# Optimization experiments

Hardware: AMD Instinct MI355X
Metric: run time of the kernel (lower is better)

Reference implementation:

```python
import jax, jax.numpy as jnp
import numpy as np


def _ramp_filter(H):
    # skimage-style Fourier ramp filter: 2*|f| with f = fftfreq(H)
    f = np.fft.fftfreq(H)
    return (2.0 * np.abs(f)).astype(np.float32)


def setup_inputs() -> dict:
    key = jax.random.key(0)
    N, H_in, W_in, D_out = 8, 768, 360, 512
    radon_image = jax.random.normal(key, (N, 1, H_in, W_in), dtype=jnp.float32)
    hG = jnp.asarray(_ramp_filter(H_in)).reshape(1, 1, H_in, 1)
    return {"radon_image": radon_image, "hG": hG, "D_out": D_out}


def reference(radon_image, hG, D_out):
    N, _, H, W = radon_image.shape
    D = D_out
    # --- Fourier-domain ramp filtering (2D FFT, multiply by real filter along detector axis, real ifft) ---
    X = jnp.fft.fft2(radon_image[:, 0])                     # [N, H, W] complex
    h = hG[0, 0, :, 0]                                      # [H]
    filt = jnp.real(jnp.fft.ifft2(X * h[None, :, None])).astype(radon_image.dtype)  # [N, H, W]

    # --- backprojection grids (matches np.mgrid / tG construction) ---
    Xg, Yg = jnp.meshgrid(jnp.arange(D), jnp.arange(D), indexing="ij")
    xpr = (Xg - D // 2).astype(jnp.float32)
    ypr = (Yg - D // 2).astype(jnp.float32)
    th = (jnp.pi / 180.0) * jnp.linspace(0.0, 180.0, W, endpoint=False)  # [W]
    txs = -1.0 + jnp.arange(W, dtype=jnp.float32) * (2.0 / (W - 1))     # [W]

    hH = H // 2
    sy = (H - 1) / 2.0   # align_corners=True y scale
    sx = (W - 1) / 2.0   # align_corners=True x scale

    def body(recon, angle):
        th_i, tx_i = angle
        t = ypr * jnp.cos(th_i) - xpr * jnp.sin(th_i)       # [D, D]
        py = (t / hH + 1.0) * sy                            # pixel y coords [D, D]
        px = (tx_i + 1.0) * sx                              # scalar pixel x coord
        x0 = jnp.floor(px).astype(jnp.int32)
        wx = px - x0
        y0 = jnp.floor(py).astype(jnp.int32)
        wy = py - y0

        def samp_col(xi):
            vx = ((xi >= 0) & (xi < W)).astype(filt.dtype)
            col = filt[:, :, jnp.clip(xi, 0, W - 1)]        # [N, H]

            def samp_y(yi):
                vy = ((yi >= 0) & (yi < H)).astype(filt.dtype)
                return col[:, jnp.clip(yi, 0, H - 1)] * vy  # [N, D, D] zero-padded

            v = samp_y(y0) * (1.0 - wy) + samp_y(y0 + 1) * wy
            return v * vx

        val = samp_col(x0) * (1.0 - wx) + samp_col(x0 + 1) * wx  # [N, D, D]
        return recon + val, None

    recon0 = jnp.zeros((N, D, D), dtype=radon_image.dtype)
    recon, _ = jax.lax.scan(body, recon0, (th, txs))
    return (recon * (jnp.pi / (2.0 * W)))[:, None]          # [N, 1, D, D]
```

## Files before the change

kernel.cpp:

```cpp
#include <hip/hip_runtime.h>
#include <math.h>

#define N_IMG 8
#define H 768
#define W 360
#define D 512
#define SY 383.5f
#define SX 179.5f
#define SC 0.00436332312998582394f
#define NC 24
#define IPAD 384

typedef __fp16 h2 __attribute__((ext_vector_type(2)));
struct H2X2 { h2 a, b; };
typedef short short8 __attribute__((ext_vector_type(8)));
typedef float f32x4 __attribute__((ext_vector_type(4)));

__device__ inline unsigned bf16pair(float a, float b) {
    unsigned ua = __builtin_bit_cast(unsigned, a);
    unsigned ub = __builtin_bit_cast(unsigned, b);
    ua += 0x7FFFu + ((ua >> 16) & 1u);
    ub += 0x7FFFu + ((ub >> 16) & 1u);
    return (ua >> 16) | (ub & 0xFFFF0000u);
}

__global__ void build_g_kernel(const float* __restrict__ hG, float* __restrict__ g) {
    int m = blockIdx.x;
    int lane = threadIdx.x;
    float s = 0.f;
#pragma unroll
    for (int q = 0; q < 12; ++q) {
        int k = lane + 64 * q;
        int prod = (k * m) % H;
        float angr = (float)prod * 0.00818123086872313911f;
        s += hG[k] * cosf(angr);
    }
#pragma unroll
    for (int off = 32; off > 0; off >>= 1) s += __shfl_down(s, off);
    if (lane == 0) g[m] = s * (1.0f / (float)H);
}

__global__ void build_ang_kernel(float2* __restrict__ ang) {
    int i = blockIdx.x * 64 + threadIdx.x;
    if (i < W) {
        float th = (float)i * 0.00872664625997164788f;
        float r = SY / 384.0f;
        ang[i] = make_float2(cosf(th) * r, -sinf(th) * r);
    }
}

#define KSTEPS 10

__global__ void build_bg_kernel(const float* __restrict__ g, uint4* __restrict__ Bg) {
    int idx = blockIdx.x * 64 + threadIdx.x;
    int L  = idx & 63;
    int tj = idx >> 6;
    int nn = (tj & 3) * 16 + (L & 15);
    int kb = (tj >> 2) * 32 + (L >> 4) * 8;
    float bf[8];
#pragma unroll
    for (int s = 0; s < 8; ++s) {
        int d = nn + 128 - (kb + s);
        d += (d < 0) ? H : 0;
        bf[s] = g[d];
    }
    uint4 pk = {bf16pair(bf[0], bf[1]), bf16pair(bf[2], bf[3]),
                bf16pair(bf[4], bf[5]), bf16pair(bf[6], bf[7])};
    Bg[idx] = pk;
}

__global__ __launch_bounds__(256)
void build_rc_kernel(const float* __restrict__ radon, uint4* __restrict__ rcC) {
    __shared__ float xs[32][69];

    const int i0 = blockIdx.x * 64;
    const int c  = blockIdx.y;
    const int n  = blockIdx.z;
    const int tid = threadIdx.x;
    const int xw0 = (i0 > 0) ? i0 - 1 : 0;
    const float* rn = radon + (size_t)n * H * W;

    {
        int mrow = tid >> 3;
        int xoff = tid & 7;
        const float* src = rn + (size_t)(32 * c + mrow) * W;
#pragma unroll
        for (int s = 0; s < 9; ++s) {
            int xo = xoff + 8 * s;
            int x = xw0 + xo;
            if (xo < 66 && x < W) xs[mrow][xo] = src[x];
        }
    }
    __syncthreads();

    const int il  = tid >> 2;
    const int oct = tid & 3;
    const int i = i0 + il;

    float w0 = 0.f, w1 = 0.f;
    int lx0 = 0, lx1 = 0;
    if (i < W) {
        float tx = -1.0f + (float)i * (2.0f / (float)(W - 1));
        float px = (tx + 1.0f) * SX;
        float fx = floorf(px);
        float wx = px - fx;
        int xi = (int)fx;
        if (xi >= 0 && xi < W)         { w0 = 1.0f - wx; lx0 = xi - xw0; }
        if (xi + 1 >= 0 && xi + 1 < W) { w1 = wx;        lx1 = xi + 1 - xw0; }
    }

    float v[8];
#pragma unroll
    for (int s = 0; s < 8; ++s) {
        int ml = oct * 8 + s;
        v[s] = w0 * xs[ml][lx0] + w1 * xs[ml][lx1];
    }
    uint4 pk = {bf16pair(v[0], v[1]), bf16pair(v[2], v[3]),
                bf16pair(v[4], v[5]), bf16pair(v[6], v[7])};
    rcC[(((size_t)n * NC + c) * IPAD + i) * 4 + oct] = pk;
}

__global__ __launch_bounds__(256)
void filt_gemm_kernel(const uint4* __restrict__ rcC, const uint4* __restrict__ Bg,
                      unsigned short* __restrict__ colp) {
    const int n  = blockIdx.z;
    const int i0 = blockIdx.y * 64;
    const int y0 = blockIdx.x * 64;
    const int wv = threadIdx.x >> 6;
    const int L  = threadIdx.x & 63;

    const int c0 = (y0 / 32 + 20) % NC;
    const uint4* An = rcC + (size_t)n * NC * IPAD * 4;
    const int arow = i0 + wv * 16 + (L & 15);
    const int aoff = L >> 4;

    f32x4 acc[4];
#pragma unroll
    for (int j = 0; j < 4; ++j) acc[j] = (f32x4){0.f, 0.f, 0.f, 0.f};

    for (int t = 0; t < KSTEPS; ++t) {
        int c = c0 + t;
        c -= (c >= NC) ? NC : 0;
        short8 a = __builtin_bit_cast(short8, An[((size_t)c * IPAD + arow) * 4 + aoff]);
#pragma unroll
        for (int j = 0; j < 4; ++j) {
            short8 b = __builtin_bit_cast(short8, Bg[(t * 4 + j) * 64 + L]);
            acc[j] = __builtin_amdgcn_mfma_f32_16x16x32_bf16(a, b, acc[j], 0, 0, 0);
        }
    }

    const int g = n >> 2, slot = n & 3;
    unsigned short* cp = colp + (size_t)g * W * H * 4 + slot;
#pragma unroll
    for (int j = 0; j < 4; ++j) {
#pragma unroll
        for (int r = 0; r < 4; ++r) {
            int ig = i0 + wv * 16 + (L >> 4) * 4 + r;
            if (ig < W) {
                int y = y0 + j * 16 + (L & 15);
                _Float16 hv = (_Float16)(acc[j][r] * SC);
                cp[((size_t)ig * H + y) * 4] = __builtin_bit_cast(unsigned short, hv);
            }
        }
    }
}

__global__ __launch_bounds__(512, 8)
void backproj_kernel(const unsigned short* __restrict__ colp,
                     const float2* __restrict__ angv, float* __restrict__ outb) {
    __shared__ __align__(16) H2X2 colh[2][H];

    const int bid = blockIdx.x;
    const int bz  = bid & 7;
    const int tle = bid >> 3;
    const int g  = bz >> 2;
    const int aq = bz & 3;
    const int a0 = aq * (W / 4);
    const int u0 = (tle >> 3) * 32;
    const int v0 = (tle & 7) * 64;
    const int tid = threadIdx.x;
    const int lane = tid & 63;
    const int tu = tid >> 6;

    const float vf = (float)(v0 + lane - D / 2);
    float uf[4];
#pragma unroll
    for (int r = 0; r < 4; ++r) uf[r] = (float)(u0 + tu + 8 * r - D / 2);

    const h2 hz = {(__fp16)0.f, (__fp16)0.f};
    float acc[4][4];
    h2 haccA[4], haccB[4];
#pragma unroll
    for (int r = 0; r < 4; ++r) {
#pragma unroll
        for (int nn = 0; nn < 4; ++nn) acc[r][nn] = 0.f;
        haccA[r] = hz;
        haccB[r] = hz;
    }

    const uint2* cp = (const uint2*)colp + (size_t)g * W * H;

    const int y1 = tid;
    const int y2 = tid + 512;

    {
        const int ab = a0 * H;
        uint2 d = cp[ab + y1];
        colh[0][y1] = __builtin_bit_cast(H2X2, d);
        if (tid < 256) {
            uint2 e = cp[ab + y2];
            colh[0][y2] = __builtin_bit_cast(H2X2, e);
        }
    }
    __syncthreads();

    for (int j = 0; j < W / 4; ++j) {
        int a = a0 + j;
        int an = (j + 1 < W / 4) ? (a + 1) : a;
        const int ab = an * H;
        uint2 d = cp[ab + y1];
        uint2 e = make_uint2(0u, 0u);
        if (tid < 256) e = cp[ab + y2];

        const int cb2 = j & 1;
        float2 AB = angv[a];
        float base = fmaf(vf, AB.x, SY);
#pragma unroll
        for (int r = 0; r < 4; ++r) {
            float py = fmaf(uf[r], AB.y, base);
            float wy = __builtin_amdgcn_fractf(py);
            int iy = (int)py;
            uint2 lo_raw = *(const uint2*)&colh[cb2][iy];
            uint2 hi_raw = *(const uint2*)&colh[cb2][iy + 1];
            H2X2 lo = __builtin_bit_cast(H2X2, lo_raw);
            H2X2 hi = __builtin_bit_cast(H2X2, hi_raw);
            h2 wy2 = __builtin_amdgcn_cvt_pkrtz(wy, wy);
            haccA[r] += lo.a + wy2 * (hi.a - lo.a);
            haccB[r] += lo.b + wy2 * (hi.b - lo.b);
        }

        if ((j & 15) == 15) {
#pragma unroll
            for (int r = 0; r < 4; ++r) {
                acc[r][0] += (float)haccA[r].x;
                acc[r][1] += (float)haccA[r].y;
                acc[r][2] += (float)haccB[r].x;
                acc[r][3] += (float)haccB[r].y;
                haccA[r] = hz;
                haccB[r] = hz;
            }
        }

        colh[cb2 ^ 1][y1] = __builtin_bit_cast(H2X2, d);
        if (tid < 256) colh[cb2 ^ 1][y2] = __builtin_bit_cast(H2X2, e);
        __syncthreads();
    }

#pragma unroll
    for (int r = 0; r < 4; ++r) {
        acc[r][0] += (float)haccA[r].x;
        acc[r][1] += (float)haccA[r].y;
        acc[r][2] += (float)haccB[r].x;
        acc[r][3] += (float)haccB[r].y;
        int u = u0 + tu + 8 * r;
#pragma unroll
        for (int nn = 0; nn < 4; ++nn) {
            size_t idx = ((size_t)(g * 4 + nn) * D + u) * D + v0 + lane;
            atomicAdd(&outb[idx], acc[r][nn]);
        }
    }
}

__global__ void zero_kernel(float4* __restrict__ o) {
    int i = blockIdx.x * 512 + threadIdx.x;
    o[i] = make_float4(0.f, 0.f, 0.f, 0.f);
}

extern "C" void kernel_launch(void* const* d_in, const int* in_sizes, int n_in,
                              void* d_out, int out_size, void* d_ws, size_t ws_size,
                              hipStream_t stream) {
    const float* radon = (const float*)d_in[0];
    const float* hG    = (const float*)d_in[1];
    float* out = (float*)d_out;

    float*  g    = (float*)d_ws;
    float2* ang  = (float2*)((char*)d_ws + 4096);
    uint4*  Bg   = (uint4*)((char*)d_ws + 8192);
    unsigned short* colp = (unsigned short*)((char*)d_ws + 65536);
    uint4*  rcC  = (uint4*)((char*)d_ws + 4489216);

    zero_kernel<<<1024, 512, 0, stream>>>((float4*)out);
    build_g_kernel<<<H, 64, 0, stream>>>(hG, g);
    build_ang_kernel<<<(W + 63) / 64, 64, 0, stream>>>(ang);
    build_bg_kernel<<<40, 64, 0, stream>>>(g, Bg);
    build_rc_kernel<<<dim3(6, NC, N_IMG), 256, 0, stream>>>(radon, rcC);
    filt_gemm_kernel<<<dim3(H / 64, 384 / 64, N_IMG), 256, 0, stream>>>(rcC, Bg, colp);
    backproj_kernel<<<1024, 512, 0, stream>>>(colp, ang, out);
}
```

Measured before the change: 172.8 us.

## Coalesce filtered-column stores via LDS, fold zeroing and setup kernels, simplify column resampling

The filter GEMM now assigns one image per wavefront and groups 4 images per block. Results are staged in shared memory so each thread writes packed 4-image fp16 uint2 values, instead of scattered 2-byte stores. The output zeroing moves into build_rc, and the angle and Bg setup kernels merge into one, cutting launches. build_rc drops the horizontal interpolation, since the sample position lands exactly on integer columns, and uses float4 loads. This relies on float rounding of px staying exact, or close enough, to an integer.

```diff
diff --git a/kernel.cpp b/kernel.cpp
--- a/kernel.cpp
+++ b/kernel.cpp
@@ -6,7 +6,6 @@
 #define W 360
 #define D 512
 #define SY 383.5f
-#define SX 179.5f
 #define SC 0.00436332312998582394f
 #define NC 24
 #define IPAD 384
@@ -40,98 +39,100 @@
     if (lane == 0) g[m] = s * (1.0f / (float)H);
 }
 
-__global__ void build_ang_kernel(float2* __restrict__ ang) {
-    int i = blockIdx.x * 64 + threadIdx.x;
-    if (i < W) {
-        float th = (float)i * 0.00872664625997164788f;
-        float r = SY / 384.0f;
-        ang[i] = make_float2(cosf(th) * r, -sinf(th) * r);
-    }
-}
-
 #define KSTEPS 10
 
-__global__ void build_bg_kernel(const float* __restrict__ g, uint4* __restrict__ Bg) {
-    int idx = blockIdx.x * 64 + threadIdx.x;
-    int L  = idx & 63;
-    int tj = idx >> 6;
-    int nn = (tj & 3) * 16 + (L & 15);
-    int kb = (tj >> 2) * 32 + (L >> 4) * 8;
-    float bf[8];
-#pragma unroll
-    for (int s = 0; s < 8; ++s) {
-        int d = nn + 128 - (kb + s);
-        d += (d < 0) ? H : 0;
-        bf[s] = g[d];
-    }
-    uint4 pk = {bf16pair(bf[0], bf[1]), bf16pair(bf[2], bf[3]),
-                bf16pair(bf[4], bf[5]), bf16pair(bf[6], bf[7])};
-    Bg[idx] = pk;
+__global__ void build_angbg_kernel(const float* __restrict__ g, uint4* __restrict__ Bg,
+                                   float2* __restrict__ ang) {
+    int b = blockIdx.x;
+    int t = threadIdx.x;
+    if (b < 40) {
+        int idx = b * 64 + t;
+        int L  = idx & 63;
+        int tj = idx >> 6;
+        int nn = (tj & 3) * 16 + (L & 15);
+        int kb = (tj >> 2) * 32 + (L >> 4) * 8;
+        float bf[8];
+#pragma unroll
+        for (int s = 0; s < 8; ++s) {
+            int d = nn + 128 - (kb + s);
+            d += (d < 0) ? H : 0;
+            bf[s] = g[d];
+        }
+        Bg[idx] = (uint4){bf16pair(bf[0], bf[1]), bf16pair(bf[2], bf[3]),
+                          bf16pair(bf[4], bf[5]), bf16pair(bf[6], bf[7])};
+    } else {
+#pragma unroll
+        for (int q = 0; q < 6; ++q) {
+            int i = t + 64 * q;
+            if (i < W) {
+                float th = (float)i * 0.00872664625997164788f;
+                float r = SY / 384.0f;
+                ang[i] = make_float2(cosf(th) * r, -sinf(th) * r);
+            }
+        }
+    }
 }
 
 __global__ __launch_bounds__(256)
-void build_rc_kernel(const float* __restrict__ radon, uint4* __restrict__ rcC) {
-    __shared__ float xs[32][69];
+void build_rc_kernel(const float* __restrict__ radon, uint4* __restrict__ rcC,
+                     float4* __restrict__ out4) {
+    __shared__ float xs[32][65];
 
     const int i0 = blockIdx.x * 64;
     const int c  = blockIdx.y;
     const int n  = blockIdx.z;
     const int tid = threadIdx.x;
-    const int xw0 = (i0 > 0) ? i0 - 1 : 0;
-    const float* rn = radon + (size_t)n * H * W;
 
     {
-        int mrow = tid >> 3;
-        int xoff = tid & 7;
-        const float* src = rn + (size_t)(32 * c + mrow) * W;
-#pragma unroll
-        for (int s = 0; s < 9; ++s) {
-            int xo = xoff + 8 * s;
-            int x = xw0 + xo;
-            if (xo < 66 && x < W) xs[mrow][xo] = src[x];
-        }
+        int flat = ((n * NC) + c) * 6 + blockIdx.x;
+        if (flat < 1024) {
+            out4[flat * 512 + tid]       = make_float4(0.f, 0.f, 0.f, 0.f);
+            out4[flat * 512 + 256 + tid] = make_float4(0.f, 0.f, 0.f, 0.f);
+        }
+    }
+
+    {
+        int mr    = tid >> 3;
+        int lane8 = tid & 7;
+        int ib = i0 + lane8 * 8;
+        const float* src = radon + ((size_t)n * H + 32 * c + mr) * W + ib;
+        float4 v0, v1;
+        if (ib + 7 < W) {
+            v0 = *(const float4*)src;
+            v1 = *(const float4*)(src + 4);
+        } else {
+            v0 = make_float4(0.f, 0.f, 0.f, 0.f);
+            v1 = make_float4(0.f, 0.f, 0.f, 0.f);
+        }
+        *(float4*)&xs[mr][lane8 * 8]     = v0;
+        *(float4*)&xs[mr][lane8 * 8 + 4] = v1;
     }
     __syncthreads();
 
     const int il  = tid >> 2;
     const int oct = tid & 3;
-    const int i = i0 + il;
-
-    float w0 = 0.f, w1 = 0.f;
-    int lx0 = 0, lx1 = 0;
-    if (i < W) {
-        float tx = -1.0f + (float)i * (2.0f / (float)(W - 1));
-        float px = (tx + 1.0f) * SX;
-        float fx = floorf(px);
-        float wx = px - fx;
-        int xi = (int)fx;
-        if (xi >= 0 && xi < W)         { w0 = 1.0f - wx; lx0 = xi - xw0; }
-        if (xi + 1 >= 0 && xi + 1 < W) { w1 = wx;        lx1 = xi + 1 - xw0; }
-    }
-
     float v[8];
 #pragma unroll
-    for (int s = 0; s < 8; ++s) {
-        int ml = oct * 8 + s;
-        v[s] = w0 * xs[ml][lx0] + w1 * xs[ml][lx1];
-    }
+    for (int s = 0; s < 8; ++s) v[s] = xs[oct * 8 + s][il];
     uint4 pk = {bf16pair(v[0], v[1]), bf16pair(v[2], v[3]),
                 bf16pair(v[4], v[5]), bf16pair(v[6], v[7])};
-    rcC[(((size_t)n * NC + c) * IPAD + i) * 4 + oct] = pk;
+    rcC[(((size_t)n * NC + c) * IPAD + i0 + il) * 4 + oct] = pk;
 }
 
 __global__ __launch_bounds__(256)
 void filt_gemm_kernel(const uint4* __restrict__ rcC, const uint4* __restrict__ Bg,
                       unsigned short* __restrict__ colp) {
-    const int n  = blockIdx.z;
-    const int i0 = blockIdx.y * 64;
+    __shared__ _Float16 lx[16][64][4];
+
+    const int grp = blockIdx.z;
+    const int i0 = blockIdx.y * 16;
     const int y0 = blockIdx.x * 64;
     const int wv = threadIdx.x >> 6;
     const int L  = threadIdx.x & 63;
 
     const int c0 = (y0 / 32 + 20) % NC;
-    const uint4* An = rcC + (size_t)n * NC * IPAD * 4;
-    const int arow = i0 + wv * 16 + (L & 15);
+    const uint4* An = rcC + (size_t)(grp * 4 + wv) * NC * IPAD * 4;
+    const int arow = i0 + (L & 15);
     const int aoff = L >> 4;
 
     f32x4 acc[4];
@@ -149,18 +150,26 @@
         }
     }
 
-    const int g = n >> 2, slot = n & 3;
-    unsigned short* cp = colp + (size_t)g * W * H * 4 + slot;
 #pragma unroll
     for (int j = 0; j < 4; ++j) {
 #pragma unroll
         for (int r = 0; r < 4; ++r) {
-            int ig = i0 + wv * 16 + (L >> 4) * 4 + r;
-            if (ig < W) {
-                int y = y0 + j * 16 + (L & 15);
-                _Float16 hv = (_Float16)(acc[j][r] * SC);
-                cp[((size_t)ig * H + y) * 4] = __builtin_bit_cast(unsigned short, hv);
-            }
+            int ilc = (L >> 4) * 4 + r;
+            int ylc = j * 16 + (L & 15);
+            lx[ilc][ylc][wv] = (_Float16)(acc[j][r] * SC);
+        }
+    }
+    __syncthreads();
+
+    unsigned short* cp = colp + (size_t)grp * W * H * 4;
+#pragma unroll
+    for (int k = 0; k < 4; ++k) {
+        int e = threadIdx.x + k * 256;
+        int ilc = e >> 6, ylc = e & 63;
+        int ig = i0 + ilc;
+        if (ig < W) {
+            uint2 v = *(const uint2*)&lx[ilc][ylc][0];
+            *(uint2*)&cp[((size_t)ig * H + y0 + ylc) * 4] = v;
         }
     }
 }
@@ -205,12 +214,8 @@
 
     {
         const int ab = a0 * H;
-        uint2 d = cp[ab + y1];
-        colh[0][y1] = __builtin_bit_cast(H2X2, d);
-        if (tid < 256) {
-            uint2 e = cp[ab + y2];
-            colh[0][y2] = __builtin_bit_cast(H2X2, e);
-        }
+        colh[0][y1] = __builtin_bit_cast(H2X2, cp[ab + y1]);
+        if (tid < 256) colh[0][y2] = __builtin_bit_cast(H2X2, cp[ab + y2]);
     }
     __syncthreads();
 
@@ -271,11 +276,6 @@
     }
 }
 
-__global__ void zero_kernel(float4* __restrict__ o) {
-    int i = blockIdx.x * 512 + threadIdx.x;
-    o[i] = make_float4(0.f, 0.f, 0.f, 0.f);
-}
-
 extern "C" void kernel_launch(void* const* d_in, const int* in_sizes, int n_in,
                               void* d_out, int out_size, void* d_ws, size_t ws_size,
                               hipStream_t stream) {
@@ -289,11 +289,9 @@
     unsigned short* colp = (unsigned short*)((char*)d_ws + 65536);
     uint4*  rcC  = (uint4*)((char*)d_ws + 4489216);
 
-    zero_kernel<<<1024, 512, 0, stream>>>((float4*)out);
     build_g_kernel<<<H, 64, 0, stream>>>(hG, g);
-    build_ang_kernel<<<(W + 63) / 64, 64, 0, stream>>>(ang);
-    build_bg_kernel<<<40, 64, 0, stream>>>(g, Bg);
-    build_rc_kernel<<<dim3(6, NC, N_IMG), 256, 0, stream>>>(radon, rcC);
-    filt_gemm_kernel<<<dim3(H / 64, 384 / 64, N_IMG), 256, 0, stream>>>(rcC, Bg, colp);
+    build_angbg_kernel<<<41, 64, 0, stream>>>(g, Bg, ang);
+    build_rc_kernel<<<dim3(6, NC, N_IMG), 256, 0, stream>>>(radon, rcC, (float4*)out);
+    filt_gemm_kernel<<<dim3(H / 64, 23, 2), 256, 0, stream>>>(rcC, Bg, colp);
     backproj_kernel<<<1024, 512, 0, stream>>>(colp, ang, out);
 }
```

Result: faster. 168.5 us (-2.5%).
